# Kernel optimization log

Measured on AMD Instinct MI355X. Metric: run time of the kernel, lower is better.

Reference implementation:

```python
import jax, jax.numpy as jnp
import numpy as np

N_NODES = 50000
N_EDGES = 800000
IN_FEAT = 256
UNITS = 128
NEG_SLOPE = 0.2  # tf.nn.leaky_relu default alpha


def setup_inputs() -> dict:
    key = jax.random.key(0)
    k1, k2, k3, k4 = jax.random.split(key, 4)
    node_states = jax.random.normal(k1, (N_NODES, IN_FEAT), dtype=jnp.float32)
    edges = jax.random.randint(k2, (N_EDGES, 2), 0, N_NODES, dtype=jnp.int64)
    kernel = jax.random.normal(k3, (IN_FEAT, UNITS), dtype=jnp.float32) * 0.05
    kernel_attention = jax.random.normal(k4, (2 * UNITS, 1), dtype=jnp.float32) * 0.05
    return {"node_states": node_states, "edges": edges,
            "kernel": kernel, "kernel_attention": kernel_attention}


def reference(node_states, edges, kernel, kernel_attention):
    # node_states: [N, F], edges: [E, 2] (col 0 = target/segment, col 1 = source)
    n_nodes = node_states.shape[0]
    tgt = edges[:, 0]
    src = edges[:, 1]

    h = node_states @ kernel  # [N, U]

    # attention score per edge: leaky_relu(concat(h[tgt], h[src]) @ a)
    # split the attention vector so the two matmuls happen per-node (same math,
    # avoids materializing the [E, 2U] concat)
    u = h.shape[1]
    a_tgt = (h @ kernel_attention[:u]).squeeze(-1)  # [N]
    a_src = (h @ kernel_attention[u:]).squeeze(-1)  # [N]
    scores = jax.nn.leaky_relu(a_tgt[tgt] + a_src[src], NEG_SLOPE)  # [E]
    scores = jnp.exp(jnp.clip(scores, -2.0, 2.0))

    # segment softmax over edges grouped by target node
    denom = jax.ops.segment_sum(scores, tgt, num_segments=n_nodes)  # [N]
    attn = scores / denom[tgt]  # [E]

    # weighted aggregation of neighbor features
    out = jax.ops.segment_sum(h[src] * attn[:, None], tgt, num_segments=n_nodes)  # [N, U]
    return out
```

## Files before the change

kernel.cpp:

```cpp
#include <hip/hip_runtime.h>
#include <hip/hip_bf16.h>

#define N_NODES 50000
#define N_EDGES 800000
#define IN_FEAT 256
#define UNITS   128
#define DEGCAP  64
#define BIN_SHIFT 6
#define BIN_TGTS  64
#define NBINS   782
#define BIN_CAP 1280
#define CHUNK   4096

typedef unsigned short ushort_t;
typedef __bf16 bf16x8 __attribute__((ext_vector_type(8)));
typedef float  f32x4  __attribute__((ext_vector_type(4)));
typedef unsigned short ushort8 __attribute__((ext_vector_type(8)));

__device__ __forceinline__ ushort_t bfbits(float f) {
    __bf16 b = (__bf16)f;
    return __builtin_bit_cast(ushort_t, b);
}

__device__ __forceinline__ void cvt8(const float4& f0, const float4& f1,
                                     ushort_t* dst) {
    bf16x8 u;
    u[0] = (__bf16)f0.x; u[1] = (__bf16)f0.y; u[2] = (__bf16)f0.z; u[3] = (__bf16)f0.w;
    u[4] = (__bf16)f1.x; u[5] = (__bf16)f1.y; u[6] = (__bf16)f1.z; u[7] = (__bf16)f1.w;
    *(bf16x8*)dst = u;
}

__global__ __launch_bounds__(256) void prep_wt_zero(const float* __restrict__ W,
                                                    ushort_t* __restrict__ Wt,
                                                    int* __restrict__ gbin) {
    int i = blockIdx.x * 256 + threadIdx.x;
    if (i < UNITS * IN_FEAT) {
        int n = i >> 8;
        int k = i & 255;
        Wt[i] = bfbits(W[(size_t)k * UNITS + n]);
    }
    if (i < 1024) gbin[i] = 0;
}

__global__ __launch_bounds__(256) void gemm_mfma(const float* __restrict__ A,
                                                 const ushort_t* __restrict__ Wt,
                                                 const float* __restrict__ ka,
                                                 ushort_t* __restrict__ Hb,
                                                 float* __restrict__ a_tgt,
                                                 float* __restrict__ a_src, int M) {
    __shared__ __align__(16) ushort_t Bs[128 * 264];
    __shared__ __align__(16) ushort_t As[2 * 64 * 40];
    __shared__ float spt[64][2];
    __shared__ float sps[64][2];
    const int tid  = threadIdx.x;
    const int lane = tid & 63;
    const int wv   = tid >> 6;
    const int wy   = wv >> 1;
    const int wx   = wv & 1;
    const int row0 = blockIdx.x * 64;
    const int quad = lane >> 4;
    const int cl   = lane & 15;

    f32x4 acc[2][4] = {};

#pragma unroll
    for (int t = 0; t < 16; ++t) {
        int j = t * 256 + tid;
        int r = j >> 5;
        int c = (j & 31) * 8;
        *(ushort8*)(Bs + r * 264 + c) = *(const ushort8*)(Wt + r * 256 + c);
    }

    const int ar = tid >> 2, aq = tid & 3;
    const int gr = min(row0 + ar, M - 1);
    const float* aptr = A + (size_t)gr * IN_FEAT + aq * 8;
    ushort_t*    asw  = As + ar * 40 + aq * 8;

    {
        float4 f0 = *(const float4*)(aptr);
        float4 f1 = *(const float4*)(aptr + 4);
        cvt8(f0, f1, asw);
    }
    __syncthreads();

    for (int kc = 0; kc < IN_FEAT; kc += 32) {
        const int cur = (kc >> 5) & 1;
        const bool more = (kc + 32 < IN_FEAT);
        float4 g0, g1;
        if (more) {
            g0 = *(const float4*)(aptr + kc + 32);
            g1 = *(const float4*)(aptr + kc + 36);
        }

        bf16x8 af[2], bff[4];
        const ushort_t* asb = As + cur * 2560;
#pragma unroll
        for (int mi = 0; mi < 2; ++mi)
            af[mi] = *(const bf16x8*)(asb + (wy * 32 + mi * 16 + cl) * 40 + quad * 8);
#pragma unroll
        for (int ni = 0; ni < 4; ++ni)
            bff[ni] = *(const bf16x8*)(Bs + (wx * 64 + ni * 16 + cl) * 264 + kc + quad * 8);
#pragma unroll
        for (int mi = 0; mi < 2; ++mi)
#pragma unroll
            for (int ni = 0; ni < 4; ++ni)
                acc[mi][ni] = __builtin_amdgcn_mfma_f32_16x16x32_bf16(
                    af[mi], bff[ni], acc[mi][ni], 0, 0, 0);

        if (more)
            cvt8(g0, g1, As + (cur ^ 1) * 2560 + ar * 40 + aq * 8);
        __syncthreads();
    }

#pragma unroll
    for (int mi = 0; mi < 2; ++mi) {
#pragma unroll
        for (int ni = 0; ni < 4; ++ni) {
            int col = wx * 64 + ni * 16 + cl;
#pragma unroll
            for (int r = 0; r < 4; ++r) {
                int row = row0 + wy * 32 + mi * 16 + quad * 4 + r;
                if (row < M)
                    Hb[(size_t)row * UNITS + col] = bfbits(acc[mi][ni][r]);
            }
        }
    }

    float kt[4], ks[4];
#pragma unroll
    for (int ni = 0; ni < 4; ++ni) {
        int col = wx * 64 + ni * 16 + cl;
        kt[ni] = ka[col];
        ks[ni] = ka[UNITS + col];
    }
#pragma unroll
    for (int mi = 0; mi < 2; ++mi) {
        float pt[4] = {}, ps[4] = {};
#pragma unroll
        for (int ni = 0; ni < 4; ++ni)
#pragma unroll
            for (int r = 0; r < 4; ++r) {
                pt[r] += acc[mi][ni][r] * kt[ni];
                ps[r] += acc[mi][ni][r] * ks[ni];
            }
#pragma unroll
        for (int r = 0; r < 4; ++r) {
#pragma unroll
            for (int m = 1; m < 16; m <<= 1) {
                pt[r] += __shfl_xor(pt[r], m);
                ps[r] += __shfl_xor(ps[r], m);
            }
            if (cl == 0) {
                int rl = wy * 32 + mi * 16 + quad * 4 + r;
                spt[rl][wx] = pt[r];
                sps[rl][wx] = ps[r];
            }
        }
    }
    __syncthreads();
    if (tid < 64) {
        int row = row0 + tid;
        if (row < M) {
            a_tgt[row] = spt[tid][0] + spt[tid][1];
            a_src[row] = sps[tid][0] + sps[tid][1];
        }
    }
}

__device__ __forceinline__ float edge_score(float at, float as) {
    float s = at + as;
    s = s > 0.f ? s : 0.2f * s;
    s = fminf(fmaxf(s, -2.f), 2.f);
    return __expf(s);
}

__global__ __launch_bounds__(1024) void bin_edges(const int* __restrict__ edges,
                                                  int* __restrict__ gbin,
                                                  int2* __restrict__ binbuf, int E) {
    __shared__ int  hist[1024];
    __shared__ int  sbase[1024];
    __shared__ int  runoff[1024];
    __shared__ int  gbase[1024];
    __shared__ int  wsum[16];
    __shared__ int2 stage[CHUNK];
    const int tid  = threadIdx.x;
    const int lane = tid & 63, wv = tid >> 6;
    const int e0   = blockIdx.x * CHUNK;

    hist[tid] = 0;
    __syncthreads();

    int2 er[4];
    int  eb[4];
#pragma unroll
    for (int j = 0; j < 4; ++j) {
        int idx = e0 + j * 1024 + tid;
        if (idx < E) {
            er[j] = ((const int2*)edges)[idx];
            eb[j] = er[j].x >> BIN_SHIFT;
            atomicAdd(&hist[eb[j]], 1);
        } else eb[j] = -1;
    }
    __syncthreads();

    int h = hist[tid];
    int incl = h;
#pragma unroll
    for (int off = 1; off < 64; off <<= 1) {
        int t = __shfl_up(incl, off);
        if (lane >= off) incl += t;
    }
    if (lane == 63) wsum[wv] = incl;
    __syncthreads();
    int excl = incl - h;
#pragma unroll
    for (int w = 0; w < 16; ++w) if (w < wv) excl += wsum[w];
    sbase[tid]  = excl;
    runoff[tid] = excl;
    __syncthreads();

    if (h > 0) gbase[tid] = atomicAdd(&gbin[tid], h);

#pragma unroll
    for (int j = 0; j < 4; ++j) {
        if (eb[j] >= 0) {
            int p = atomicAdd(&runoff[eb[j]], 1);
            stage[p] = er[j];
        }
    }
    __syncthreads();

    int total = sbase[1023] + hist[1023];
    for (int p = tid; p < total; p += 1024) {
        int2 ts = stage[p];
        int b   = ts.x >> BIN_SHIFT;
        int dst = gbase[b] + (p - sbase[b]);
        if (dst < BIN_CAP)
            binbuf[(size_t)b * BIN_CAP + dst] = ts;
    }
}

__global__ __launch_bounds__(512) void scatter_aggregate(
        const int2* __restrict__ binbuf, const int* __restrict__ gbin,
        const float* __restrict__ at, const float* __restrict__ as,
        const ushort_t* __restrict__ Hb, float* __restrict__ out, int M) {
    __shared__ int2  lcsr[BIN_CAP];
    __shared__ int   lcnt[BIN_TGTS];
    __shared__ int   loff[BIN_TGTS];
    __shared__ int   roff[BIN_TGTS];
    __shared__ float atl[BIN_TGTS];
    const int tid = threadIdx.x;
    const int bin = blockIdx.x;
    const int t0  = bin << BIN_SHIFT;
    if (tid < BIN_TGTS) {
        lcnt[tid] = 0;
        int t = t0 + tid;
        atl[tid] = (t < M) ? at[t] : 0.f;
    }
    __syncthreads();

    const int bcnt = min(gbin[bin], BIN_CAP);
    const int2* src = binbuf + (size_t)bin * BIN_CAP;

    for (int p = tid; p < bcnt; p += 512) {
        int2 ts = src[p];
        atomicAdd(&lcnt[ts.x - t0], 1);
    }
    __syncthreads();

    if (tid < 64) {
        int h = lcnt[tid];
        int incl = h;
#pragma unroll
        for (int off = 1; off < 64; off <<= 1) {
            int t = __shfl_up(incl, off);
            if (tid >= off) incl += t;
        }
        loff[tid] = incl - h;
        roff[tid] = incl - h;
    }
    __syncthreads();

    for (int p = tid; p < bcnt; p += 512) {
        int2 ts = src[p];
        int lt  = ts.x - t0;
        float sc = edge_score(atl[lt], as[ts.y]);
        int r = atomicAdd(&roff[lt], 1);
        lcsr[r] = make_int2(ts.y, __float_as_int(sc));
    }
    __syncthreads();

    const int lane = tid & 63;
    const int wv   = tid >> 6;
    const int g    = lane >> 4;
    const int c    = lane & 15;

#pragma unroll
    for (int ln = 0; ln < 8; ln += 2) {
        const int ltA = wv * 8 + ln;
        const int ltB = ltA + 1;
        const int begA = loff[ltA], degA = min(lcnt[ltA], DEGCAP);
        const int begB = loff[ltB], degB = min(lcnt[ltB], DEGCAP);

        float accA[8] = {}, accB[8] = {};
        float wsA = 0.f, wsB = 0.f;
        const int ns = (max(degA, degB) + 3) >> 2;
        for (int t = 0; t < ns; ++t) {
            const int slot = t * 4 + g;
            int2 swA = (slot < degA) ? lcsr[begA + slot] : make_int2(0, 0);
            int2 swB = (slot < degB) ? lcsr[begB + slot] : make_int2(0, 0);
            float wA = __int_as_float(swA.y);
            float wB = __int_as_float(swB.y);
            uint4 uA = *(const uint4*)(Hb + (size_t)swA.x * UNITS + c * 8);
            uint4 uB = *(const uint4*)(Hb + (size_t)swB.x * UNITS + c * 8);
            wsA += wA; wsB += wB;
            accA[0] += wA * __uint_as_float(uA.x << 16);
            accA[1] += wA * __uint_as_float(uA.x & 0xffff0000u);
            accA[2] += wA * __uint_as_float(uA.y << 16);
            accA[3] += wA * __uint_as_float(uA.y & 0xffff0000u);
            accA[4] += wA * __uint_as_float(uA.z << 16);
            accA[5] += wA * __uint_as_float(uA.z & 0xffff0000u);
            accA[6] += wA * __uint_as_float(uA.w << 16);
            accA[7] += wA * __uint_as_float(uA.w & 0xffff0000u);
            accB[0] += wB * __uint_as_float(uB.x << 16);
            accB[1] += wB * __uint_as_float(uB.x & 0xffff0000u);
            accB[2] += wB * __uint_as_float(uB.y << 16);
            accB[3] += wB * __uint_as_float(uB.y & 0xffff0000u);
            accB[4] += wB * __uint_as_float(uB.z << 16);
            accB[5] += wB * __uint_as_float(uB.z & 0xffff0000u);
            accB[6] += wB * __uint_as_float(uB.w << 16);
            accB[7] += wB * __uint_as_float(uB.w & 0xffff0000u);
        }

#pragma unroll
        for (int i = 0; i < 8; ++i) {
            accA[i] += __shfl_xor(accA[i], 16);
            accA[i] += __shfl_xor(accA[i], 32);
            accB[i] += __shfl_xor(accB[i], 16);
            accB[i] += __shfl_xor(accB[i], 32);
        }
        wsA += __shfl_xor(wsA, 16); wsA += __shfl_xor(wsA, 32);
        wsB += __shfl_xor(wsB, 16); wsB += __shfl_xor(wsB, 32);
        const float scA = (degA > 0) ? 1.0f / wsA : 0.0f;
        const float scB = (degB > 0) ? 1.0f / wsB : 0.0f;

        if (g == 0) {
            const int nodeA = t0 + ltA;
            const int nodeB = t0 + ltB;
            if (nodeA < M) {
                float* dst = out + (size_t)nodeA * UNITS + c * 8;
                *(float4*)dst       = make_float4(accA[0] * scA, accA[1] * scA,
                                                  accA[2] * scA, accA[3] * scA);
                *(float4*)(dst + 4) = make_float4(accA[4] * scA, accA[5] * scA,
                                                  accA[6] * scA, accA[7] * scA);
            }
            if (nodeB < M) {
                float* dst = out + (size_t)nodeB * UNITS + c * 8;
                *(float4*)dst       = make_float4(accB[0] * scB, accB[1] * scB,
                                                  accB[2] * scB, accB[3] * scB);
                *(float4*)(dst + 4) = make_float4(accB[4] * scB, accB[5] * scB,
                                                  accB[6] * scB, accB[7] * scB);
            }
        }
    }
}

extern "C" void kernel_launch(void* const* d_in, const int* in_sizes, int n_in,
                              void* d_out, int out_size, void* d_ws, size_t ws_size,
                              hipStream_t stream) {
    const float* node_states = (const float*)d_in[0];
    const int*   edges       = (const int*)d_in[1];
    const float* W           = (const float*)d_in[2];
    const float* ka          = (const float*)d_in[3];
    float*       out         = (float*)d_out;

    const int M = N_NODES, E = N_EDGES;

    ushort_t* hb     = (ushort_t*)d_ws;
    float*    a_tgt  = (float*)(hb + (size_t)M * UNITS);
    float*    a_src  = a_tgt + M;
    int*      gbin   = (int*)(a_src + M);
    int2*     binbuf = (int2*)(gbin + 1024);
    ushort_t* wt     = (ushort_t*)binbuf;

    const int nblkA = (E + CHUNK - 1) / CHUNK;

    prep_wt_zero    <<<(UNITS * IN_FEAT + 255) / 256, 256, 0, stream>>>(W, wt, gbin);
    gemm_mfma       <<<(M + 63) / 64, 256, 0, stream>>>(node_states, wt, ka, hb,
                                                        a_tgt, a_src, M);
    bin_edges       <<<nblkA, 1024, 0, stream>>>(edges, gbin, binbuf, E);
    scatter_aggregate<<<NBINS, 512, 0, stream>>>(binbuf, gbin, a_tgt, a_src,
                                                 hb, out, M);
}
```

Before: 156.4 us.

## Fuse GEMM and edge binning into one launch and prefetch gathers in aggregation

The GEMM and edge-binning kernels now run as a single launch. Block index picks the role, so the two independent phases run side by side on the GPU and one launch plus its serial dependency go away. Binning blocks drop to 256 threads, each handling 16 edges, with a 4-bins-per-thread scan. The Wt buffer moves so it no longer aliases binbuf, because both phases are now live at the same time. The aggregation loop also software-prefetches the next neighbour's CSR entry and H row to hide gather latency, at the cost of more registers.

```diff
diff --git a/kernel.cpp b/kernel.cpp
--- a/kernel.cpp
+++ b/kernel.cpp
@@ -11,6 +11,8 @@
 #define NBINS   782
 #define BIN_CAP 1280
 #define CHUNK   4096
+#define GEMM_BLOCKS 782
+#define BIN_BLOCKS  196
 
 typedef unsigned short ushort_t;
 typedef __bf16 bf16x8 __attribute__((ext_vector_type(8)));
@@ -42,131 +44,6 @@
     if (i < 1024) gbin[i] = 0;
 }
 
-__global__ __launch_bounds__(256) void gemm_mfma(const float* __restrict__ A,
-                                                 const ushort_t* __restrict__ Wt,
-                                                 const float* __restrict__ ka,
-                                                 ushort_t* __restrict__ Hb,
-                                                 float* __restrict__ a_tgt,
-                                                 float* __restrict__ a_src, int M) {
-    __shared__ __align__(16) ushort_t Bs[128 * 264];
-    __shared__ __align__(16) ushort_t As[2 * 64 * 40];
-    __shared__ float spt[64][2];
-    __shared__ float sps[64][2];
-    const int tid  = threadIdx.x;
-    const int lane = tid & 63;
-    const int wv   = tid >> 6;
-    const int wy   = wv >> 1;
-    const int wx   = wv & 1;
-    const int row0 = blockIdx.x * 64;
-    const int quad = lane >> 4;
-    const int cl   = lane & 15;
-
-    f32x4 acc[2][4] = {};
-
-#pragma unroll
-    for (int t = 0; t < 16; ++t) {
-        int j = t * 256 + tid;
-        int r = j >> 5;
-        int c = (j & 31) * 8;
-        *(ushort8*)(Bs + r * 264 + c) = *(const ushort8*)(Wt + r * 256 + c);
-    }
-
-    const int ar = tid >> 2, aq = tid & 3;
-    const int gr = min(row0 + ar, M - 1);
-    const float* aptr = A + (size_t)gr * IN_FEAT + aq * 8;
-    ushort_t*    asw  = As + ar * 40 + aq * 8;
-
-    {
-        float4 f0 = *(const float4*)(aptr);
-        float4 f1 = *(const float4*)(aptr + 4);
-        cvt8(f0, f1, asw);
-    }
-    __syncthreads();
-
-    for (int kc = 0; kc < IN_FEAT; kc += 32) {
-        const int cur = (kc >> 5) & 1;
-        const bool more = (kc + 32 < IN_FEAT);
-        float4 g0, g1;
-        if (more) {
-            g0 = *(const float4*)(aptr + kc + 32);
-            g1 = *(const float4*)(aptr + kc + 36);
-        }
-
-        bf16x8 af[2], bff[4];
-        const ushort_t* asb = As + cur * 2560;
-#pragma unroll
-        for (int mi = 0; mi < 2; ++mi)
-            af[mi] = *(const bf16x8*)(asb + (wy * 32 + mi * 16 + cl) * 40 + quad * 8);
-#pragma unroll
-        for (int ni = 0; ni < 4; ++ni)
-            bff[ni] = *(const bf16x8*)(Bs + (wx * 64 + ni * 16 + cl) * 264 + kc + quad * 8);
-#pragma unroll
-        for (int mi = 0; mi < 2; ++mi)
-#pragma unroll
-            for (int ni = 0; ni < 4; ++ni)
-                acc[mi][ni] = __builtin_amdgcn_mfma_f32_16x16x32_bf16(
-                    af[mi], bff[ni], acc[mi][ni], 0, 0, 0);
-
-        if (more)
-            cvt8(g0, g1, As + (cur ^ 1) * 2560 + ar * 40 + aq * 8);
-        __syncthreads();
-    }
-
-#pragma unroll
-    for (int mi = 0; mi < 2; ++mi) {
-#pragma unroll
-        for (int ni = 0; ni < 4; ++ni) {
-            int col = wx * 64 + ni * 16 + cl;
-#pragma unroll
-            for (int r = 0; r < 4; ++r) {
-                int row = row0 + wy * 32 + mi * 16 + quad * 4 + r;
-                if (row < M)
-                    Hb[(size_t)row * UNITS + col] = bfbits(acc[mi][ni][r]);
-            }
-        }
-    }
-
-    float kt[4], ks[4];
-#pragma unroll
-    for (int ni = 0; ni < 4; ++ni) {
-        int col = wx * 64 + ni * 16 + cl;
-        kt[ni] = ka[col];
-        ks[ni] = ka[UNITS + col];
-    }
-#pragma unroll
-    for (int mi = 0; mi < 2; ++mi) {
-        float pt[4] = {}, ps[4] = {};
-#pragma unroll
-        for (int ni = 0; ni < 4; ++ni)
-#pragma unroll
-            for (int r = 0; r < 4; ++r) {
-                pt[r] += acc[mi][ni][r] * kt[ni];
-                ps[r] += acc[mi][ni][r] * ks[ni];
-            }
-#pragma unroll
-        for (int r = 0; r < 4; ++r) {
-#pragma unroll
-            for (int m = 1; m < 16; m <<= 1) {
-                pt[r] += __shfl_xor(pt[r], m);
-                ps[r] += __shfl_xor(ps[r], m);
-            }
-            if (cl == 0) {
-                int rl = wy * 32 + mi * 16 + quad * 4 + r;
-                spt[rl][wx] = pt[r];
-                sps[rl][wx] = ps[r];
-            }
-        }
-    }
-    __syncthreads();
-    if (tid < 64) {
-        int row = row0 + tid;
-        if (row < M) {
-            a_tgt[row] = spt[tid][0] + spt[tid][1];
-            a_src[row] = sps[tid][0] + sps[tid][1];
-        }
-    }
-}
-
 __device__ __forceinline__ float edge_score(float at, float as) {
     float s = at + as;
     s = s > 0.f ? s : 0.2f * s;
@@ -174,69 +51,207 @@
     return __expf(s);
 }
 
-__global__ __launch_bounds__(1024) void bin_edges(const int* __restrict__ edges,
-                                                  int* __restrict__ gbin,
-                                                  int2* __restrict__ binbuf, int E) {
-    __shared__ int  hist[1024];
-    __shared__ int  sbase[1024];
-    __shared__ int  runoff[1024];
-    __shared__ int  gbase[1024];
-    __shared__ int  wsum[16];
-    __shared__ int2 stage[CHUNK];
+__global__ __launch_bounds__(256) void gemm_bin(
+        const float* __restrict__ A, const ushort_t* __restrict__ Wt,
+        const float* __restrict__ ka, const int* __restrict__ edges,
+        int* __restrict__ gbin, int2* __restrict__ binbuf,
+        ushort_t* __restrict__ Hb, float* __restrict__ a_tgt,
+        float* __restrict__ a_src, int M, int E) {
+    __shared__ __align__(16) char smem[78848];
     const int tid  = threadIdx.x;
-    const int lane = tid & 63, wv = tid >> 6;
-    const int e0   = blockIdx.x * CHUNK;
-
-    hist[tid] = 0;
-    __syncthreads();
-
-    int2 er[4];
-    int  eb[4];
-#pragma unroll
-    for (int j = 0; j < 4; ++j) {
-        int idx = e0 + j * 1024 + tid;
-        if (idx < E) {
-            er[j] = ((const int2*)edges)[idx];
-            eb[j] = er[j].x >> BIN_SHIFT;
-            atomicAdd(&hist[eb[j]], 1);
-        } else eb[j] = -1;
-    }
-    __syncthreads();
-
-    int h = hist[tid];
-    int incl = h;
-#pragma unroll
-    for (int off = 1; off < 64; off <<= 1) {
-        int t = __shfl_up(incl, off);
-        if (lane >= off) incl += t;
-    }
-    if (lane == 63) wsum[wv] = incl;
-    __syncthreads();
-    int excl = incl - h;
-#pragma unroll
-    for (int w = 0; w < 16; ++w) if (w < wv) excl += wsum[w];
-    sbase[tid]  = excl;
-    runoff[tid] = excl;
-    __syncthreads();
-
-    if (h > 0) gbase[tid] = atomicAdd(&gbin[tid], h);
-
-#pragma unroll
-    for (int j = 0; j < 4; ++j) {
-        if (eb[j] >= 0) {
-            int p = atomicAdd(&runoff[eb[j]], 1);
-            stage[p] = er[j];
-        }
-    }
-    __syncthreads();
-
-    int total = sbase[1023] + hist[1023];
-    for (int p = tid; p < total; p += 1024) {
-        int2 ts = stage[p];
-        int b   = ts.x >> BIN_SHIFT;
-        int dst = gbase[b] + (p - sbase[b]);
-        if (dst < BIN_CAP)
-            binbuf[(size_t)b * BIN_CAP + dst] = ts;
+    const int lane = tid & 63;
+    const int wv   = tid >> 6;
+
+    if (blockIdx.x < GEMM_BLOCKS) {
+        ushort_t* Bs = (ushort_t*)smem;
+        ushort_t* As = Bs + 128 * 264;
+        float (*spt)[2] = (float(*)[2])(As + 2 * 64 * 40);
+        float (*sps)[2] = spt + 64;
+        const int wy   = wv >> 1;
+        const int wx   = wv & 1;
+        const int row0 = blockIdx.x * 64;
+        const int quad = lane >> 4;
+        const int cl   = lane & 15;
+
+        f32x4 acc[2][4] = {};
+
+#pragma unroll
+        for (int t = 0; t < 16; ++t) {
+            int j = t * 256 + tid;
+            int r = j >> 5;
+            int c = (j & 31) * 8;
+            *(ushort8*)(Bs + r * 264 + c) = *(const ushort8*)(Wt + r * 256 + c);
+        }
+
+        const int ar = tid >> 2, aq = tid & 3;
+        const int gr = min(row0 + ar, M - 1);
+        const float* aptr = A + (size_t)gr * IN_FEAT + aq * 8;
+        ushort_t*    asw  = As + ar * 40 + aq * 8;
+
+        {
+            float4 f0 = *(const float4*)(aptr);
+            float4 f1 = *(const float4*)(aptr + 4);
+            cvt8(f0, f1, asw);
+        }
+        __syncthreads();
+
+        for (int kc = 0; kc < IN_FEAT; kc += 32) {
+            const int cur = (kc >> 5) & 1;
+            const bool more = (kc + 32 < IN_FEAT);
+            float4 g0, g1;
+            if (more) {
+                g0 = *(const float4*)(aptr + kc + 32);
+                g1 = *(const float4*)(aptr + kc + 36);
+            }
+
+            bf16x8 af[2], bff[4];
+            const ushort_t* asb = As + cur * 2560;
+#pragma unroll
+            for (int mi = 0; mi < 2; ++mi)
+                af[mi] = *(const bf16x8*)(asb + (wy * 32 + mi * 16 + cl) * 40 + quad * 8);
+#pragma unroll
+            for (int ni = 0; ni < 4; ++ni)
+                bff[ni] = *(const bf16x8*)(Bs + (wx * 64 + ni * 16 + cl) * 264 + kc + quad * 8);
+#pragma unroll
+            for (int mi = 0; mi < 2; ++mi)
+#pragma unroll
+                for (int ni = 0; ni < 4; ++ni)
+                    acc[mi][ni] = __builtin_amdgcn_mfma_f32_16x16x32_bf16(
+                        af[mi], bff[ni], acc[mi][ni], 0, 0, 0);
+
+            if (more)
+                cvt8(g0, g1, As + (cur ^ 1) * 2560 + ar * 40 + aq * 8);
+            __syncthreads();
+        }
+
+#pragma unroll
+        for (int mi = 0; mi < 2; ++mi) {
+#pragma unroll
+            for (int ni = 0; ni < 4; ++ni) {
+                int col = wx * 64 + ni * 16 + cl;
+#pragma unroll
+                for (int r = 0; r < 4; ++r) {
+                    int row = row0 + wy * 32 + mi * 16 + quad * 4 + r;
+                    if (row < M)
+                        Hb[(size_t)row * UNITS + col] = bfbits(acc[mi][ni][r]);
+                }
+            }
+        }
+
+        float kt[4], ks[4];
+#pragma unroll
+        for (int ni = 0; ni < 4; ++ni) {
+            int col = wx * 64 + ni * 16 + cl;
+            kt[ni] = ka[col];
+            ks[ni] = ka[UNITS + col];
+        }
+#pragma unroll
+        for (int mi = 0; mi < 2; ++mi) {
+            float pt[4] = {}, ps[4] = {};
+#pragma unroll
+            for (int ni = 0; ni < 4; ++ni)
+#pragma unroll
+                for (int r = 0; r < 4; ++r) {
+                    pt[r] += acc[mi][ni][r] * kt[ni];
+                    ps[r] += acc[mi][ni][r] * ks[ni];
+                }
+#pragma unroll
+            for (int r = 0; r < 4; ++r) {
+#pragma unroll
+                for (int m = 1; m < 16; m <<= 1) {
+                    pt[r] += __shfl_xor(pt[r], m);
+                    ps[r] += __shfl_xor(ps[r], m);
+                }
+                if (cl == 0) {
+                    int rl = wy * 32 + mi * 16 + quad * 4 + r;
+                    spt[rl][wx] = pt[r];
+                    sps[rl][wx] = ps[r];
+                }
+            }
+        }
+        __syncthreads();
+        if (tid < 64) {
+            int row = row0 + tid;
+            if (row < M) {
+                a_tgt[row] = spt[tid][0] + spt[tid][1];
+                a_src[row] = sps[tid][0] + sps[tid][1];
+            }
+        }
+    } else {
+        int*  hist   = (int*)smem;
+        int*  sbase  = hist + 1024;
+        int*  runoff = sbase + 1024;
+        int*  gbase  = runoff + 1024;
+        int*  wsum4  = gbase + 1024;
+        int2* stage  = (int2*)(smem + 16400);
+        const int e0 = (blockIdx.x - GEMM_BLOCKS) * CHUNK;
+
+#pragma unroll
+        for (int j = 0; j < 4; ++j) hist[j * 256 + tid] = 0;
+        __syncthreads();
+
+        int2 er[16];
+        int  eb[16];
+#pragma unroll
+        for (int j = 0; j < 16; ++j) {
+            int idx = e0 + j * 256 + tid;
+            if (idx < E) {
+                er[j] = ((const int2*)edges)[idx];
+                eb[j] = er[j].x >> BIN_SHIFT;
+                atomicAdd(&hist[eb[j]], 1);
+            } else eb[j] = -1;
+        }
+        __syncthreads();
+
+        int h[4];
+        int s = 0;
+#pragma unroll
+        for (int i = 0; i < 4; ++i) { h[i] = hist[4 * tid + i]; s += h[i]; }
+        int incl = s;
+#pragma unroll
+        for (int off = 1; off < 64; off <<= 1) {
+            int t = __shfl_up(incl, off);
+            if (lane >= off) incl += t;
+        }
+        if (lane == 63) wsum4[wv] = incl;
+        __syncthreads();
+        int excl = incl - s;
+#pragma unroll
+        for (int w = 0; w < 4; ++w) if (w < wv) excl += wsum4[w];
+        {
+            int r = excl;
+#pragma unroll
+            for (int i = 0; i < 4; ++i) {
+                sbase[4 * tid + i]  = r;
+                runoff[4 * tid + i] = r;
+                r += h[i];
+            }
+        }
+        __syncthreads();
+
+#pragma unroll
+        for (int i = 0; i < 4; ++i) {
+            int b = 4 * tid + i;
+            if (h[i] > 0) gbase[b] = atomicAdd(&gbin[b], h[i]);
+        }
+
+#pragma unroll
+        for (int j = 0; j < 16; ++j) {
+            if (eb[j] >= 0) {
+                int p = atomicAdd(&runoff[eb[j]], 1);
+                stage[p] = er[j];
+            }
+        }
+        __syncthreads();
+
+        int total = min(CHUNK, E - e0);
+        for (int p = tid; p < total; p += 256) {
+            int2 ts = stage[p];
+            int b   = ts.x >> BIN_SHIFT;
+            int dst = gbase[b] + (p - sbase[b]);
+            if (dst < BIN_CAP)
+                binbuf[(size_t)b * BIN_CAP + dst] = ts;
+        }
     }
 }
 
@@ -305,31 +320,40 @@
         float accA[8] = {}, accB[8] = {};
         float wsA = 0.f, wsB = 0.f;
         const int ns = (max(degA, degB) + 3) >> 2;
+
+        int2 cA = (g < degA) ? lcsr[begA + g] : make_int2(0, 0);
+        int2 cB = (g < degB) ? lcsr[begB + g] : make_int2(0, 0);
+        uint4 cuA = *(const uint4*)(Hb + (size_t)cA.x * UNITS + c * 8);
+        uint4 cuB = *(const uint4*)(Hb + (size_t)cB.x * UNITS + c * 8);
+
         for (int t = 0; t < ns; ++t) {
-            const int slot = t * 4 + g;
-            int2 swA = (slot < degA) ? lcsr[begA + slot] : make_int2(0, 0);
-            int2 swB = (slot < degB) ? lcsr[begB + slot] : make_int2(0, 0);
-            float wA = __int_as_float(swA.y);
-            float wB = __int_as_float(swB.y);
-            uint4 uA = *(const uint4*)(Hb + (size_t)swA.x * UNITS + c * 8);
-            uint4 uB = *(const uint4*)(Hb + (size_t)swB.x * UNITS + c * 8);
+            const int sl1 = (t + 1) * 4 + g;
+            int2 nA = (t + 1 < ns && sl1 < degA) ? lcsr[begA + sl1] : make_int2(0, 0);
+            int2 nB = (t + 1 < ns && sl1 < degB) ? lcsr[begB + sl1] : make_int2(0, 0);
+            uint4 nuA = *(const uint4*)(Hb + (size_t)nA.x * UNITS + c * 8);
+            uint4 nuB = *(const uint4*)(Hb + (size_t)nB.x * UNITS + c * 8);
+
+            const float wA = __int_as_float(cA.y);
+            const float wB = __int_as_float(cB.y);
             wsA += wA; wsB += wB;
-            accA[0] += wA * __uint_as_float(uA.x << 16);
-            accA[1] += wA * __uint_as_float(uA.x & 0xffff0000u);
-            accA[2] += wA * __uint_as_float(uA.y << 16);
-            accA[3] += wA * __uint_as_float(uA.y & 0xffff0000u);
-            accA[4] += wA * __uint_as_float(uA.z << 16);
-            accA[5] += wA * __uint_as_float(uA.z & 0xffff0000u);
-            accA[6] += wA * __uint_as_float(uA.w << 16);
-            accA[7] += wA * __uint_as_float(uA.w & 0xffff0000u);
-            accB[0] += wB * __uint_as_float(uB.x << 16);
-            accB[1] += wB * __uint_as_float(uB.x & 0xffff0000u);
-            accB[2] += wB * __uint_as_float(uB.y << 16);
-            accB[3] += wB * __uint_as_float(uB.y & 0xffff0000u);
-            accB[4] += wB * __uint_as_float(uB.z << 16);
-            accB[5] += wB * __uint_as_float(uB.z & 0xffff0000u);
-            accB[6] += wB * __uint_as_float(uB.w << 16);
-            accB[7] += wB * __uint_as_float(uB.w & 0xffff0000u);
+            accA[0] += wA * __uint_as_float(cuA.x << 16);
+            accA[1] += wA * __uint_as_float(cuA.x & 0xffff0000u);
+            accA[2] += wA * __uint_as_float(cuA.y << 16);
+            accA[3] += wA * __uint_as_float(cuA.y & 0xffff0000u);
+            accA[4] += wA * __uint_as_float(cuA.z << 16);
+            accA[5] += wA * __uint_as_float(cuA.z & 0xffff0000u);
+            accA[6] += wA * __uint_as_float(cuA.w << 16);
+            accA[7] += wA * __uint_as_float(cuA.w & 0xffff0000u);
+            accB[0] += wB * __uint_as_float(cuB.x << 16);
+            accB[1] += wB * __uint_as_float(cuB.x & 0xffff0000u);
+            accB[2] += wB * __uint_as_float(cuB.y << 16);
+            accB[3] += wB * __uint_as_float(cuB.y & 0xffff0000u);
+            accB[4] += wB * __uint_as_float(cuB.z << 16);
+            accB[5] += wB * __uint_as_float(cuB.z & 0xffff0000u);
+            accB[6] += wB * __uint_as_float(cuB.w << 16);
+            accB[7] += wB * __uint_as_float(cuB.w & 0xffff0000u);
+
+            cA = nA; cB = nB; cuA = nuA; cuB = nuB;
         }
 
 #pragma unroll
@@ -381,14 +405,12 @@
     float*    a_src  = a_tgt + M;
     int*      gbin   = (int*)(a_src + M);
     int2*     binbuf = (int2*)(gbin + 1024);
-    ushort_t* wt     = (ushort_t*)binbuf;
-
-    const int nblkA = (E + CHUNK - 1) / CHUNK;
+    ushort_t* wt     = (ushort_t*)(binbuf + (size_t)NBINS * BIN_CAP);
 
     prep_wt_zero    <<<(UNITS * IN_FEAT + 255) / 256, 256, 0, stream>>>(W, wt, gbin);
-    gemm_mfma       <<<(M + 63) / 64, 256, 0, stream>>>(node_states, wt, ka, hb,
-                                                        a_tgt, a_src, M);
-    bin_edges       <<<nblkA, 1024, 0, stream>>>(edges, gbin, binbuf, E);
+    gemm_bin        <<<GEMM_BLOCKS + BIN_BLOCKS, 256, 0, stream>>>(
+                        node_states, wt, ka, edges, gbin, binbuf,
+                        hb, a_tgt, a_src, M, E);
     scatter_aggregate<<<NBINS, 512, 0, stream>>>(binbuf, gbin, a_tgt, a_src,
                                                  hb, out, M);
 }
```

New measurement: 160.0 us. 2.3% more time.

## Deepen GEMM A-prefetch to three stages and pad global bin counters

Applied to the files above, without the earlier changes.

The GEMM A-tile loading is restructured into a fully unrolled loop that keeps three K-chunks of global loads in flight in registers, not one, so global latency is hidden behind more MFMA work. Separately, the per-bin global atomic counters are spaced GPAD ints apart to reduce contention and false sharing between neighbouring bins. The bf16 weight transpose buffer is also moved out of the binbuf region so the two no longer alias. This costs extra registers, which could lower occupancy, and a somewhat larger workspace with a larger zeroing pass.

```diff
diff --git a/kernel.cpp b/kernel.cpp
--- a/kernel.cpp
+++ b/kernel.cpp
@@ -11,6 +11,7 @@
 #define NBINS   782
 #define BIN_CAP 1280
 #define CHUNK   4096
+#define GPAD    16
 
 typedef unsigned short ushort_t;
 typedef __bf16 bf16x8 __attribute__((ext_vector_type(8)));
@@ -39,7 +40,14 @@
         int k = i & 255;
         Wt[i] = bfbits(W[(size_t)k * UNITS + n]);
     }
-    if (i < 1024) gbin[i] = 0;
+    if (i < 1024 * GPAD) gbin[i] = 0;
+}
+
+__device__ __forceinline__ float edge_score(float at, float as) {
+    float s = at + as;
+    s = s > 0.f ? s : 0.2f * s;
+    s = fminf(fmaxf(s, -2.f), 2.f);
+    return __expf(s);
 }
 
 __global__ __launch_bounds__(256) void gemm_mfma(const float* __restrict__ A,
@@ -74,26 +82,26 @@
     const int ar = tid >> 2, aq = tid & 3;
     const int gr = min(row0 + ar, M - 1);
     const float* aptr = A + (size_t)gr * IN_FEAT + aq * 8;
-    ushort_t*    asw  = As + ar * 40 + aq * 8;
-
-    {
-        float4 f0 = *(const float4*)(aptr);
-        float4 f1 = *(const float4*)(aptr + 4);
-        cvt8(f0, f1, asw);
-    }
-    __syncthreads();
-
-    for (int kc = 0; kc < IN_FEAT; kc += 32) {
-        const int cur = (kc >> 5) & 1;
-        const bool more = (kc + 32 < IN_FEAT);
-        float4 g0, g1;
-        if (more) {
-            g0 = *(const float4*)(aptr + kc + 32);
-            g1 = *(const float4*)(aptr + kc + 36);
+    ushort_t* aw0 = As + ar * 40 + aq * 8;
+    ushort_t* aw1 = As + 2560 + ar * 40 + aq * 8;
+
+    float4 pa[3], pb[3];
+    pa[0] = *(const float4*)(aptr);       pb[0] = *(const float4*)(aptr + 4);
+    pa[1] = *(const float4*)(aptr + 32);  pb[1] = *(const float4*)(aptr + 36);
+    pa[2] = *(const float4*)(aptr + 64);  pb[2] = *(const float4*)(aptr + 68);
+    cvt8(pa[0], pb[0], aw0);
+    __syncthreads();
+
+#pragma unroll
+    for (int s = 0; s < 8; ++s) {
+        const int kc = s * 32;
+        if (s + 3 < 8) {
+            pa[s % 3] = *(const float4*)(aptr + kc + 96);
+            pb[s % 3] = *(const float4*)(aptr + kc + 100);
         }
 
         bf16x8 af[2], bff[4];
-        const ushort_t* asb = As + cur * 2560;
+        const ushort_t* asb = As + (s & 1) * 2560;
 #pragma unroll
         for (int mi = 0; mi < 2; ++mi)
             af[mi] = *(const bf16x8*)(asb + (wy * 32 + mi * 16 + cl) * 40 + quad * 8);
@@ -107,8 +115,8 @@
                 acc[mi][ni] = __builtin_amdgcn_mfma_f32_16x16x32_bf16(
                     af[mi], bff[ni], acc[mi][ni], 0, 0, 0);
 
-        if (more)
-            cvt8(g0, g1, As + (cur ^ 1) * 2560 + ar * 40 + aq * 8);
+        if (s + 1 < 8)
+            cvt8(pa[(s + 1) % 3], pb[(s + 1) % 3], (s & 1) ? aw0 : aw1);
         __syncthreads();
     }
 
@@ -165,13 +173,6 @@
             a_src[row] = sps[tid][0] + sps[tid][1];
         }
     }
-}
-
-__device__ __forceinline__ float edge_score(float at, float as) {
-    float s = at + as;
-    s = s > 0.f ? s : 0.2f * s;
-    s = fminf(fmaxf(s, -2.f), 2.f);
-    return __expf(s);
 }
 
 __global__ __launch_bounds__(1024) void bin_edges(const int* __restrict__ edges,
@@ -219,7 +220,7 @@
     runoff[tid] = excl;
     __syncthreads();
 
-    if (h > 0) gbase[tid] = atomicAdd(&gbin[tid], h);
+    if (h > 0) gbase[tid] = atomicAdd(&gbin[tid * GPAD], h);
 
 #pragma unroll
     for (int j = 0; j < 4; ++j) {
@@ -259,7 +260,7 @@
     }
     __syncthreads();
 
-    const int bcnt = min(gbin[bin], BIN_CAP);
+    const int bcnt = min(gbin[bin * GPAD], BIN_CAP);
     const int2* src = binbuf + (size_t)bin * BIN_CAP;
 
     for (int p = tid; p < bcnt; p += 512) {
@@ -380,15 +381,15 @@
     float*    a_tgt  = (float*)(hb + (size_t)M * UNITS);
     float*    a_src  = a_tgt + M;
     int*      gbin   = (int*)(a_src + M);
-    int2*     binbuf = (int2*)(gbin + 1024);
-    ushort_t* wt     = (ushort_t*)binbuf;
-
-    const int nblkA = (E + CHUNK - 1) / CHUNK;
+    int2*     binbuf = (int2*)(gbin + 1024 * GPAD);
+    ushort_t* wt     = (ushort_t*)(binbuf + (size_t)NBINS * BIN_CAP);
+
+    const int nblkB = (E + CHUNK - 1) / CHUNK;
 
     prep_wt_zero    <<<(UNITS * IN_FEAT + 255) / 256, 256, 0, stream>>>(W, wt, gbin);
     gemm_mfma       <<<(M + 63) / 64, 256, 0, stream>>>(node_states, wt, ka, hb,
                                                         a_tgt, a_src, M);
-    bin_edges       <<<nblkA, 1024, 0, stream>>>(edges, gbin, binbuf, E);
+    bin_edges       <<<nblkB, 1024, 0, stream>>>(edges, gbin, binbuf, E);
     scatter_aggregate<<<NBINS, 512, 0, stream>>>(binbuf, gbin, a_tgt, a_src,
                                                  hb, out, M);
 }
```

Measured after the change: 156.4 us. Within noise of the previous version (+0.0%).
